# Optimization experiments

Hardware: AMD Instinct MI355X
Metric: run time of the kernel (lower is better)

Reference implementation:

```python
import jax, jax.numpy as jnp
import numpy as np

TEMP = 0.07
LAMBDA_INFONCE = 1.0
LAMBDA_NTXENT = 0.5
EPS = 1e-8

B, S, H, C = 32, 2048, 1024, 5


def _l2norm(x):
    # F.normalize-style row L2 normalization
    n = jnp.sqrt(jnp.sum(x * x, axis=1, keepdims=True))
    return x / jnp.maximum(n, 1e-12)


def _proj(x, W1, b1, W2, b2):
    h = jax.nn.relu(x @ W1 + b1)
    return _l2norm(h @ W2 + b2)


def setup_inputs() -> dict:
    key = jax.random.key(0)
    ks = jax.random.split(key, 12)
    sc1 = 1.0 / np.sqrt(H)
    sc2 = 1.0 / np.sqrt(H // 2)
    sc3 = 1.0 / np.sqrt(2 * H)
    return {
        "span_features": jax.random.normal(ks[0], (B, S, H), jnp.float32),
        "aspect_logits": jax.random.normal(ks[1], (B, S, C), jnp.float32),
        "opinion_logits": jax.random.normal(ks[2], (B, S, C), jnp.float32),
        "sentiment_labels": jax.random.randint(ks[3], (B,), 0, 3),
        "Wa1": jax.random.normal(ks[4], (H, H // 2), jnp.float32) * sc1,
        "ba1": jnp.zeros((H // 2,), jnp.float32),
        "Wa2": jax.random.normal(ks[5], (H // 2, 128), jnp.float32) * sc2,
        "ba2": jnp.zeros((128,), jnp.float32),
        "Wo1": jax.random.normal(ks[6], (H, H // 2), jnp.float32) * sc1,
        "bo1": jnp.zeros((H // 2,), jnp.float32),
        "Wo2": jax.random.normal(ks[7], (H // 2, 128), jnp.float32) * sc2,
        "bo2": jnp.zeros((128,), jnp.float32),
        "Ws1": jax.random.normal(ks[8], (2 * H, H), jnp.float32) * sc3,
        "bs1": jnp.zeros((H,), jnp.float32),
        "Ws2": jax.random.normal(ks[9], (H, 256), jnp.float32) * sc1,
        "bs2": jnp.zeros((256,), jnp.float32),
    }


def _pool(span_features, logits):
    # attention pooling: softmax over seq of summed non-O class logits
    w = jax.nn.softmax(logits[:, :, 1:].sum(axis=-1), axis=-1)  # [B, S]
    return jnp.einsum("bsh,bs->bh", span_features, w)  # [B, H]


def _infonce(a, o, labels):
    n = a.shape[0]
    sim = (a @ o.T) / TEMP  # [B, B]
    same = labels[:, None] == labels[None, :]
    eye = jnp.eye(n, dtype=a.dtype)
    pos_mask = eye + 0.5 * (same & (eye == 0)).astype(a.dtype)
    exp_sim = jnp.exp(sim)
    return -jnp.mean(jnp.log((exp_sim * pos_mask).sum(1) / exp_sim.sum(1) + EPS))


def _ntxent(s, labels):
    n = s.shape[0]
    s = _l2norm(s)
    sim = (s @ s.T) / TEMP
    same = (labels[:, None] == labels[None, :]).astype(s.dtype)
    mask = same - jnp.eye(n, dtype=s.dtype)
    exp_sim = jnp.exp(sim)
    pos = (exp_sim * mask).sum(1)
    neg = (exp_sim * (1.0 - mask)).sum(1)
    pos_count = mask.sum(1)
    has_pos = pos_count > 0
    row = jnp.where(has_pos,
                    -jnp.log(pos / (pos + neg) + EPS) / jnp.maximum(pos_count, 1.0),
                    0.0)
    return row.sum() / jnp.maximum(has_pos.sum(), 1).astype(s.dtype)


def reference(span_features, aspect_logits, opinion_logits, sentiment_labels,
              Wa1, ba1, Wa2, ba2, Wo1, bo1, Wo2, bo2, Ws1, bs1, Ws2, bs2):
    a_emb = _pool(span_features, aspect_logits)   # [B, H]
    o_emb = _pool(span_features, opinion_logits)  # [B, H]
    a_proj = _proj(a_emb, Wa1, ba1, Wa2, ba2)     # [B, 128]
    o_proj = _proj(o_emb, Wo1, bo1, Wo2, bo2)     # [B, 128]
    infonce = _infonce(a_proj, o_proj, sentiment_labels)
    s_proj = _proj(jnp.concatenate([a_emb, o_emb], axis=-1), Ws1, bs1, Ws2, bs2)
    ntxent = _ntxent(s_proj, sentiment_labels)
    # generation_embeddings is None -> cross_modal_loss = 0
    return LAMBDA_INFONCE * infonce + LAMBDA_NTXENT * ntxent
```

## Files before the change

### kernel.cpp

```cpp
#include <hip/hip_runtime.h>
#include <hip/hip_bf16.h>

#define BB 32
#define SS 2048
#define HH 1024
#define CC 5
#define TEMP_INV (1.0f/0.07f)

__global__ void pool_weights(const float* __restrict__ alog,
                             const float* __restrict__ olog,
                             float* __restrict__ w_a,
                             float* __restrict__ w_o) {
    int b = blockIdx.x >> 1;
    int which = blockIdx.x & 1;
    const float* lg = which ? olog : alog;
    float* wout = which ? w_o : w_a;
    __shared__ float raw[SS * CC];
    __shared__ float sl[SS];
    __shared__ float red[256];
    int t = threadIdx.x;
    const float4* src = (const float4*)(lg + (size_t)b * SS * CC);
    float4* dst = (float4*)raw;
    for (int i = t; i < SS * CC / 4; i += 256) dst[i] = src[i];
    __syncthreads();
    for (int s = t; s < SS; s += 256) {
        int base = s * 5;
        sl[s] = raw[base + 1] + raw[base + 2] + raw[base + 3] + raw[base + 4];
    }
    __syncthreads();
    float m = -1e30f;
    for (int s = t; s < SS; s += 256) m = fmaxf(m, sl[s]);
    red[t] = m;
    __syncthreads();
    for (int o = 128; o > 0; o >>= 1) {
        if (t < o) red[t] = fmaxf(red[t], red[t + o]);
        __syncthreads();
    }
    m = red[0];
    __syncthreads();
    float sum = 0.f;
    for (int s = t; s < SS; s += 256) {
        float e = expf(sl[s] - m);
        sl[s] = e;
        sum += e;
    }
    red[t] = sum;
    __syncthreads();
    for (int o = 128; o > 0; o >>= 1) {
        if (t < o) red[t] += red[t + o];
        __syncthreads();
    }
    float inv = 1.0f / red[0];
    for (int s = t; s < SS; s += 256) wout[(size_t)b * SS + s] = sl[s] * inv;
}

__global__ void pool_partial(const float* __restrict__ span,
                             const float* __restrict__ w_a,
                             const float* __restrict__ w_o,
                             float* __restrict__ part_a,
                             float* __restrict__ part_o) {
    int b = blockIdx.x >> 5;
    int chunk = blockIdx.x & 31;
    int t = threadIdx.x;
    __shared__ float wa[64], wo[64];
    int s0 = chunk * 64;
    if (t < 64) {
        wa[t] = w_a[(size_t)b * SS + s0 + t];
        wo[t] = w_o[(size_t)b * SS + s0 + t];
    }
    __syncthreads();
    const float4* sp = (const float4*)span + ((size_t)b * SS + s0) * (HH / 4) + t;
    float4 aa = {0.f, 0.f, 0.f, 0.f};
    float4 oo = {0.f, 0.f, 0.f, 0.f};
    #pragma unroll 8
    for (int ss = 0; ss < 64; ++ss) {
        float4 v = sp[(size_t)ss * (HH / 4)];
        float fa = wa[ss], fo = wo[ss];
        aa.x += v.x * fa; aa.y += v.y * fa; aa.z += v.z * fa; aa.w += v.w * fa;
        oo.x += v.x * fo; oo.y += v.y * fo; oo.z += v.z * fo; oo.w += v.w * fo;
    }
    size_t idx = ((size_t)chunk * BB + b) * HH + (size_t)t * 4;
    *(float4*)(part_a + idx) = aa;
    *(float4*)(part_o + idx) = oo;
}

__global__ void pool_reduce(const float* __restrict__ part_a,
                            const float* __restrict__ part_o,
                            float* __restrict__ a_emb,
                            float* __restrict__ o_emb) {
    int gid = blockIdx.x * 256 + threadIdx.x;
    int which = gid >> 15;
    int r = gid & 32767;
    const float* p = which ? part_o : part_a;
    float s = 0.f;
    #pragma unroll
    for (int c = 0; c < 32; ++c) s += p[(size_t)c * 32768 + r];
    (which ? o_emb : a_emb)[r] = s;
}

__global__ void gemm1_all(const float* __restrict__ a_emb, const float* __restrict__ o_emb,
                          const float* __restrict__ Wa1, const float* __restrict__ Wo1,
                          const float* __restrict__ Ws1,
                          float* __restrict__ p1_a, float* __restrict__ p1_o,
                          float* __restrict__ p1_s) {
    int bid = blockIdx.x;
    const float* xp; const float* W; float* part; int N, kb, jb;
    if (bid < 32) {
        jb = bid & 7; kb = bid >> 3; N = 512; W = Wa1; part = p1_a;
        xp = a_emb + kb * 256;
    } else if (bid < 64) {
        int r = bid - 32;
        jb = r & 7; kb = r >> 3; N = 512; W = Wo1; part = p1_o;
        xp = o_emb + kb * 256;
    } else {
        int r = bid - 64;
        jb = r & 15; kb = r >> 4; N = 1024; W = Ws1; part = p1_s;
        int kk0 = kb * 256;
        xp = (kk0 < 1024) ? (a_emb + kk0) : (o_emb + (kk0 - 1024));
    }
    int k0 = kb * 256;
    __shared__ float xs[32][256];
    int t = threadIdx.x;
    #pragma unroll
    for (int i = 0; i < 8; ++i) {
        int f = t + i * 256;
        int b = f >> 6;
        int kk = (f & 63) * 4;
        *(float4*)(&xs[b][kk]) = *(const float4*)(xp + (size_t)b * HH + kk);
    }
    __syncthreads();
    int jl = t & 63, bg = t >> 6;
    int j = jb * 64 + jl;
    float acc[8] = {0.f, 0.f, 0.f, 0.f, 0.f, 0.f, 0.f, 0.f};
    const float* Wp = W + (size_t)k0 * N + j;
    for (int k = 0; k < 256; k += 4) {
        float w0 = Wp[(size_t)(k + 0) * N];
        float w1 = Wp[(size_t)(k + 1) * N];
        float w2 = Wp[(size_t)(k + 2) * N];
        float w3 = Wp[(size_t)(k + 3) * N];
        #pragma unroll
        for (int bi = 0; bi < 8; ++bi) {
            float4 xv = *(const float4*)(&xs[bg * 8 + bi][k]);
            acc[bi] += xv.x * w0 + xv.y * w1 + xv.z * w2 + xv.w * w3;
        }
    }
    float* pp = part + (size_t)kb * 32 * N + j;
    #pragma unroll
    for (int bi = 0; bi < 8; ++bi)
        pp[(size_t)(bg * 8 + bi) * N] = acc[bi];
}

__global__ void layer2_all(const float* __restrict__ p1_a, const float* __restrict__ ba1,
                           const float* __restrict__ Wa2, const float* __restrict__ ba2,
                           const float* __restrict__ p1_o, const float* __restrict__ bo1,
                           const float* __restrict__ Wo2, const float* __restrict__ bo2,
                           const float* __restrict__ p1_s, const float* __restrict__ bs1,
                           const float* __restrict__ Ws2, const float* __restrict__ bs2,
                           float* __restrict__ a_proj, float* __restrict__ o_proj,
                           float* __restrict__ s_proj) {
    __shared__ float x[1024];
    __shared__ float red[256];
    int bid = blockIdx.x;
    int t = threadIdx.x;
    if (bid < 64) {
        int which = bid >> 5;
        int b = bid & 31;
        const float* part = which ? p1_o : p1_a;
        const float* b1 = which ? bo1 : ba1;
        const float* W2 = which ? Wo2 : Wa2;
        const float* b2 = which ? bo2 : ba2;
        float* out = (which ? o_proj : a_proj) + (size_t)b * 128;
        for (int j = t; j < 512; j += 256) {
            float s = b1[j];
            #pragma unroll
            for (int kb = 0; kb < 4; ++kb) s += part[(size_t)kb * 32 * 512 + (size_t)b * 512 + j];
            x[j] = fmaxf(s, 0.f);
        }
        __syncthreads();
        float acc = 0.f;
        if (t < 128) {
            acc = b2[t];
            for (int k = 0; k < 512; ++k) acc += x[k] * W2[(size_t)k * 128 + t];
        }
        red[t] = (t < 128) ? acc * acc : 0.f;
        __syncthreads();
        for (int o = 128; o > 0; o >>= 1) {
            if (t < o) red[t] += red[t + o];
            __syncthreads();
        }
        float n = fmaxf(sqrtf(red[0]), 1e-12f);
        if (t < 128) out[t] = acc / n;
    } else {
        int b = bid - 64;
        for (int j = t; j < 1024; j += 256) {
            float s = bs1[j];
            #pragma unroll
            for (int kb = 0; kb < 8; ++kb) s += p1_s[(size_t)kb * 32 * 1024 + (size_t)b * 1024 + j];
            x[j] = fmaxf(s, 0.f);
        }
        __syncthreads();
        float acc = bs2[t];
        for (int k = 0; k < 1024; ++k) acc += x[k] * Ws2[(size_t)k * 256 + t];
        red[t] = acc * acc;
        __syncthreads();
        for (int o = 128; o > 0; o >>= 1) {
            if (t < o) red[t] += red[t + o];
            __syncthreads();
        }
        float n = fmaxf(sqrtf(red[0]), 1e-12f);
        s_proj[(size_t)b * 256 + t] = acc / n;
    }
}

__global__ void loss_kernel(const float* __restrict__ a_proj,
                            const float* __restrict__ o_proj,
                            const float* __restrict__ s_proj,
                            const int* __restrict__ labels,
                            float* __restrict__ out) {
    __shared__ float ap[BB * 128];
    __shared__ float op[BB * 128];
    __shared__ float sp[BB * 256];
    __shared__ float rowv[BB], rownt[BB];
    __shared__ int hp[BB], lab[BB];
    int t = threadIdx.x;
    for (int i = t; i < BB * 128; i += 1024) { ap[i] = a_proj[i]; op[i] = o_proj[i]; }
    for (int i = t; i < BB * 256; i += 1024) sp[i] = s_proj[i];
    if (t < BB) lab[t] = labels[t];
    __syncthreads();
    int i = t >> 5, j = t & 31;

    float ssq = 0.f;
    for (int k = 0; k < 8; ++k) {
        float v = sp[i * 256 + j * 8 + k];
        ssq += v * v;
    }
    for (int m = 16; m > 0; m >>= 1) ssq += __shfl_xor(ssq, m, 64);
    float inv = 1.0f / fmaxf(sqrtf(ssq), 1e-12f);
    for (int k = j; k < 256; k += 32) sp[i * 256 + k] *= inv;
    __syncthreads();

    float dot = 0.f;
    for (int k = 0; k < 128; ++k) dot += ap[i * 128 + k] * op[j * 128 + k];
    float e = expf(dot * TEMP_INV);
    float maskv = (i == j) ? 1.0f : ((lab[i] == lab[j]) ? 0.5f : 0.0f);
    float num = e * maskv, den = e;
    for (int m = 16; m > 0; m >>= 1) {
        num += __shfl_xor(num, m, 64);
        den += __shfl_xor(den, m, 64);
    }

    float dn = 0.f;
    for (int k = 0; k < 256; ++k) dn += sp[i * 256 + k] * sp[j * 256 + k];
    float en = expf(dn * TEMP_INV);
    float mnt = (lab[i] == lab[j]) ? ((i == j) ? 0.f : 1.f) : 0.f;
    float pos = en * mnt, neg = en * (1.f - mnt), pc = mnt;
    for (int m = 16; m > 0; m >>= 1) {
        pos += __shfl_xor(pos, m, 64);
        neg += __shfl_xor(neg, m, 64);
        pc += __shfl_xor(pc, m, 64);
    }

    if (j == 0) {
        rowv[i] = -logf(num / den + 1e-8f);
        bool has = pc > 0.f;
        rownt[i] = has ? (-logf(pos / (pos + neg) + 1e-8f) / fmaxf(pc, 1.0f)) : 0.f;
        hp[i] = has ? 1 : 0;
    }
    __syncthreads();
    if (t == 0) {
        float inf = 0.f, nt = 0.f;
        int h = 0;
        for (int q = 0; q < BB; ++q) { inf += rowv[q]; nt += rownt[q]; h += hp[q]; }
        inf /= (float)BB;
        nt /= (float)(h > 0 ? h : 1);
        out[0] = 1.0f * inf + 0.5f * nt;
    }
}

extern "C" void kernel_launch(void* const* d_in, const int* in_sizes, int n_in,
                              void* d_out, int out_size, void* d_ws, size_t ws_size,
                              hipStream_t stream) {
    const float* span  = (const float*)d_in[0];
    const float* alog  = (const float*)d_in[1];
    const float* olog  = (const float*)d_in[2];
    const int*   labs  = (const int*)d_in[3];
    const float* Wa1   = (const float*)d_in[4];
    const float* ba1   = (const float*)d_in[5];
    const float* Wa2   = (const float*)d_in[6];
    const float* ba2   = (const float*)d_in[7];
    const float* Wo1   = (const float*)d_in[8];
    const float* bo1   = (const float*)d_in[9];
    const float* Wo2   = (const float*)d_in[10];
    const float* bo2   = (const float*)d_in[11];
    const float* Ws1   = (const float*)d_in[12];
    const float* bs1   = (const float*)d_in[13];
    const float* Ws2   = (const float*)d_in[14];
    const float* bs2   = (const float*)d_in[15];

    float* ws = (float*)d_ws;
    float* w_a    = ws;
    float* w_o    = ws + 65536;
    float* part_a = ws + 131072;
    float* part_o = ws + 1179648;
    float* a_emb  = ws + 2228224;
    float* o_emb  = ws + 2260992;
    float* p1_a   = ws + 2293760;
    float* p1_o   = ws + 2359296;
    float* p1_s   = ws + 2424832;
    float* a_proj = ws + 2686976;
    float* o_proj = ws + 2691072;
    float* s_proj = ws + 2695168;

    hipLaunchKernelGGL(pool_weights, dim3(64), dim3(256), 0, stream, alog, olog, w_a, w_o);
    hipLaunchKernelGGL(pool_partial, dim3(1024), dim3(256), 0, stream,
                       span, w_a, w_o, part_a, part_o);
    hipLaunchKernelGGL(pool_reduce, dim3(256), dim3(256), 0, stream,
                       part_a, part_o, a_emb, o_emb);
    hipLaunchKernelGGL(gemm1_all, dim3(192), dim3(256), 0, stream,
                       a_emb, o_emb, Wa1, Wo1, Ws1, p1_a, p1_o, p1_s);
    hipLaunchKernelGGL(layer2_all, dim3(96), dim3(256), 0, stream,
                       p1_a, ba1, Wa2, ba2, p1_o, bo1, Wo2, bo2,
                       p1_s, bs1, Ws2, bs2, a_proj, o_proj, s_proj);
    hipLaunchKernelGGL(loss_kernel, dim3(1), dim3(1024), 0, stream,
                       a_proj, o_proj, s_proj, labs, (float*)d_out);
}
```

Before: 531.0 us.

## Split tail GEMMs finer across more threads and pad loss-kernel shared arrays

The first projection GEMM now uses K-chunks of 128 instead of 256 with 512-thread blocks and twice as many blocks, so more CUs work on the weight reads. The second layer splits the K dimension across thread groups and combines them in shared memory. The loss kernel pads its shared arrays to avoid bank conflicts in the row-dot loops. All of this targets the small tail kernels, while the dominant cost is the span pooling pass, which is unchanged.

```diff
diff --git a/kernel.cpp b/kernel.cpp
--- a/kernel.cpp
+++ b/kernel.cpp
@@ -7,7 +7,7 @@
 #define CC 5
 #define TEMP_INV (1.0f/0.07f)
 
-__global__ void pool_weights(const float* __restrict__ alog,
+__global__ __launch_bounds__(256) void pool_weights(const float* __restrict__ alog,
                              const float* __restrict__ olog,
                              float* __restrict__ w_a,
                              float* __restrict__ w_o) {
@@ -54,7 +54,7 @@
     for (int s = t; s < SS; s += 256) wout[(size_t)b * SS + s] = sl[s] * inv;
 }
 
-__global__ void pool_partial(const float* __restrict__ span,
+__global__ __launch_bounds__(256) void pool_partial(const float* __restrict__ span,
                              const float* __restrict__ w_a,
                              const float* __restrict__ w_o,
                              float* __restrict__ part_a,
@@ -84,7 +84,7 @@
     *(float4*)(part_o + idx) = oo;
 }
 
-__global__ void pool_reduce(const float* __restrict__ part_a,
+__global__ __launch_bounds__(256) void pool_reduce(const float* __restrict__ part_a,
                             const float* __restrict__ part_o,
                             float* __restrict__ a_emb,
                             float* __restrict__ o_emb) {
@@ -98,59 +98,59 @@
     (which ? o_emb : a_emb)[r] = s;
 }
 
-__global__ void gemm1_all(const float* __restrict__ a_emb, const float* __restrict__ o_emb,
+__global__ __launch_bounds__(512) void gemm1_all(const float* __restrict__ a_emb, const float* __restrict__ o_emb,
                           const float* __restrict__ Wa1, const float* __restrict__ Wo1,
                           const float* __restrict__ Ws1,
                           float* __restrict__ p1_a, float* __restrict__ p1_o,
                           float* __restrict__ p1_s) {
     int bid = blockIdx.x;
     const float* xp; const float* W; float* part; int N, kb, jb;
-    if (bid < 32) {
+    if (bid < 64) {
         jb = bid & 7; kb = bid >> 3; N = 512; W = Wa1; part = p1_a;
-        xp = a_emb + kb * 256;
-    } else if (bid < 64) {
-        int r = bid - 32;
+        xp = a_emb + kb * 128;
+    } else if (bid < 128) {
+        int r = bid - 64;
         jb = r & 7; kb = r >> 3; N = 512; W = Wo1; part = p1_o;
-        xp = o_emb + kb * 256;
+        xp = o_emb + kb * 128;
     } else {
-        int r = bid - 64;
+        int r = bid - 128;
         jb = r & 15; kb = r >> 4; N = 1024; W = Ws1; part = p1_s;
-        int kk0 = kb * 256;
+        int kk0 = kb * 128;
         xp = (kk0 < 1024) ? (a_emb + kk0) : (o_emb + (kk0 - 1024));
     }
-    int k0 = kb * 256;
-    __shared__ float xs[32][256];
+    int k0 = kb * 128;
+    __shared__ float xs[32][128];
     int t = threadIdx.x;
     #pragma unroll
-    for (int i = 0; i < 8; ++i) {
-        int f = t + i * 256;
-        int b = f >> 6;
-        int kk = (f & 63) * 4;
+    for (int i = 0; i < 2; ++i) {
+        int f = t + i * 512;
+        int b = f >> 5;
+        int kk = (f & 31) * 4;
         *(float4*)(&xs[b][kk]) = *(const float4*)(xp + (size_t)b * HH + kk);
     }
     __syncthreads();
     int jl = t & 63, bg = t >> 6;
     int j = jb * 64 + jl;
-    float acc[8] = {0.f, 0.f, 0.f, 0.f, 0.f, 0.f, 0.f, 0.f};
+    float acc[4] = {0.f, 0.f, 0.f, 0.f};
     const float* Wp = W + (size_t)k0 * N + j;
-    for (int k = 0; k < 256; k += 4) {
+    for (int k = 0; k < 128; k += 4) {
         float w0 = Wp[(size_t)(k + 0) * N];
         float w1 = Wp[(size_t)(k + 1) * N];
         float w2 = Wp[(size_t)(k + 2) * N];
         float w3 = Wp[(size_t)(k + 3) * N];
         #pragma unroll
-        for (int bi = 0; bi < 8; ++bi) {
-            float4 xv = *(const float4*)(&xs[bg * 8 + bi][k]);
+        for (int bi = 0; bi < 4; ++bi) {
+            float4 xv = *(const float4*)(&xs[bg * 4 + bi][k]);
             acc[bi] += xv.x * w0 + xv.y * w1 + xv.z * w2 + xv.w * w3;
         }
     }
     float* pp = part + (size_t)kb * 32 * N + j;
     #pragma unroll
-    for (int bi = 0; bi < 8; ++bi)
-        pp[(size_t)(bg * 8 + bi) * N] = acc[bi];
-}
-
-__global__ void layer2_all(const float* __restrict__ p1_a, const float* __restrict__ ba1,
+    for (int bi = 0; bi < 4; ++bi)
+        pp[(size_t)(bg * 4 + bi) * N] = acc[bi];
+}
+
+__global__ __launch_bounds__(512) void layer2_all(const float* __restrict__ p1_a, const float* __restrict__ ba1,
                            const float* __restrict__ Wa2, const float* __restrict__ ba2,
                            const float* __restrict__ p1_o, const float* __restrict__ bo1,
                            const float* __restrict__ Wo2, const float* __restrict__ bo2,
@@ -159,7 +159,7 @@
                            float* __restrict__ a_proj, float* __restrict__ o_proj,
                            float* __restrict__ s_proj) {
     __shared__ float x[1024];
-    __shared__ float red[256];
+    __shared__ float red[512];
     int bid = blockIdx.x;
     int t = threadIdx.x;
     if (bid < 64) {
@@ -170,77 +170,96 @@
         const float* W2 = which ? Wo2 : Wa2;
         const float* b2 = which ? bo2 : ba2;
         float* out = (which ? o_proj : a_proj) + (size_t)b * 128;
-        for (int j = t; j < 512; j += 256) {
-            float s = b1[j];
+        {
+            float s = b1[t];
             #pragma unroll
-            for (int kb = 0; kb < 4; ++kb) s += part[(size_t)kb * 32 * 512 + (size_t)b * 512 + j];
+            for (int kb = 0; kb < 8; ++kb) s += part[(size_t)kb * 32 * 512 + (size_t)b * 512 + t];
+            x[t] = fmaxf(s, 0.f);
+        }
+        __syncthreads();
+        int jj = t & 127, kh = t >> 7;
+        float acc = (kh == 0) ? b2[jj] : 0.f;
+        const float* Wc = W2 + jj;
+        for (int k = kh * 128; k < kh * 128 + 128; ++k) acc += x[k] * Wc[(size_t)k * 128];
+        red[t] = acc;
+        __syncthreads();
+        float tot = 0.f;
+        if (t < 128) tot = red[t] + red[t + 128] + red[t + 256] + red[t + 384];
+        __syncthreads();
+        if (t < 128) red[t] = tot * tot;
+        __syncthreads();
+        for (int o = 64; o > 0; o >>= 1) {
+            if (t < o) red[t] += red[t + o];
+            __syncthreads();
+        }
+        float n = fmaxf(sqrtf(red[0]), 1e-12f);
+        if (t < 128) out[t] = tot / n;
+    } else {
+        int b = bid - 64;
+        for (int j = t; j < 1024; j += 512) {
+            float s = bs1[j];
+            #pragma unroll
+            for (int kb = 0; kb < 16; ++kb) s += p1_s[(size_t)kb * 32 * 1024 + (size_t)b * 1024 + j];
             x[j] = fmaxf(s, 0.f);
         }
         __syncthreads();
-        float acc = 0.f;
-        if (t < 128) {
-            acc = b2[t];
-            for (int k = 0; k < 512; ++k) acc += x[k] * W2[(size_t)k * 128 + t];
-        }
-        red[t] = (t < 128) ? acc * acc : 0.f;
+        int jj = t & 255, kh = t >> 8;
+        float acc = (kh == 0) ? bs2[jj] : 0.f;
+        const float* Wc = Ws2 + jj;
+        for (int k = kh * 512; k < kh * 512 + 512; ++k) acc += x[k] * Wc[(size_t)k * 256];
+        red[t] = acc;
+        __syncthreads();
+        float tot = 0.f;
+        if (t < 256) tot = red[t] + red[t + 256];
+        __syncthreads();
+        if (t < 256) red[t] = tot * tot;
         __syncthreads();
         for (int o = 128; o > 0; o >>= 1) {
             if (t < o) red[t] += red[t + o];
             __syncthreads();
         }
         float n = fmaxf(sqrtf(red[0]), 1e-12f);
-        if (t < 128) out[t] = acc / n;
-    } else {
-        int b = bid - 64;
-        for (int j = t; j < 1024; j += 256) {
-            float s = bs1[j];
-            #pragma unroll
-            for (int kb = 0; kb < 8; ++kb) s += p1_s[(size_t)kb * 32 * 1024 + (size_t)b * 1024 + j];
-            x[j] = fmaxf(s, 0.f);
-        }
-        __syncthreads();
-        float acc = bs2[t];
-        for (int k = 0; k < 1024; ++k) acc += x[k] * Ws2[(size_t)k * 256 + t];
-        red[t] = acc * acc;
-        __syncthreads();
-        for (int o = 128; o > 0; o >>= 1) {
-            if (t < o) red[t] += red[t + o];
-            __syncthreads();
-        }
-        float n = fmaxf(sqrtf(red[0]), 1e-12f);
-        s_proj[(size_t)b * 256 + t] = acc / n;
-    }
-}
-
-__global__ void loss_kernel(const float* __restrict__ a_proj,
+        if (t < 256) s_proj[(size_t)b * 256 + t] = tot / n;
+    }
+}
+
+__global__ __launch_bounds__(1024) void loss_kernel(const float* __restrict__ a_proj,
                             const float* __restrict__ o_proj,
                             const float* __restrict__ s_proj,
                             const int* __restrict__ labels,
                             float* __restrict__ out) {
-    __shared__ float ap[BB * 128];
-    __shared__ float op[BB * 128];
-    __shared__ float sp[BB * 256];
+    __shared__ float ap[BB][129];
+    __shared__ float op[BB][129];
+    __shared__ float sp[BB][257];
     __shared__ float rowv[BB], rownt[BB];
     __shared__ int hp[BB], lab[BB];
     int t = threadIdx.x;
-    for (int i = t; i < BB * 128; i += 1024) { ap[i] = a_proj[i]; op[i] = o_proj[i]; }
-    for (int i = t; i < BB * 256; i += 1024) sp[i] = s_proj[i];
+    for (int idx = t; idx < BB * 128; idx += 1024) {
+        int r = idx >> 7, c = idx & 127;
+        ap[r][c] = a_proj[idx];
+        op[r][c] = o_proj[idx];
+    }
+    for (int idx = t; idx < BB * 256; idx += 1024) {
+        int r = idx >> 8, c = idx & 255;
+        sp[r][c] = s_proj[idx];
+    }
     if (t < BB) lab[t] = labels[t];
     __syncthreads();
     int i = t >> 5, j = t & 31;
 
     float ssq = 0.f;
+    #pragma unroll
     for (int k = 0; k < 8; ++k) {
-        float v = sp[i * 256 + j * 8 + k];
+        float v = sp[i][j * 8 + k];
         ssq += v * v;
     }
     for (int m = 16; m > 0; m >>= 1) ssq += __shfl_xor(ssq, m, 64);
     float inv = 1.0f / fmaxf(sqrtf(ssq), 1e-12f);
-    for (int k = j; k < 256; k += 32) sp[i * 256 + k] *= inv;
+    for (int k = j; k < 256; k += 32) sp[i][k] *= inv;
     __syncthreads();
 
     float dot = 0.f;
-    for (int k = 0; k < 128; ++k) dot += ap[i * 128 + k] * op[j * 128 + k];
+    for (int k = 0; k < 128; ++k) dot += ap[i][k] * op[j][k];
     float e = expf(dot * TEMP_INV);
     float maskv = (i == j) ? 1.0f : ((lab[i] == lab[j]) ? 0.5f : 0.0f);
     float num = e * maskv, den = e;
@@ -250,7 +269,7 @@
     }
 
     float dn = 0.f;
-    for (int k = 0; k < 256; ++k) dn += sp[i * 256 + k] * sp[j * 256 + k];
+    for (int k = 0; k < 256; ++k) dn += sp[i][k] * sp[j][k];
     float en = expf(dn * TEMP_INV);
     float mnt = (lab[i] == lab[j]) ? ((i == j) ? 0.f : 1.f) : 0.f;
     float pos = en * mnt, neg = en * (1.f - mnt), pc = mnt;
@@ -305,20 +324,20 @@
     float* a_emb  = ws + 2228224;
     float* o_emb  = ws + 2260992;
     float* p1_a   = ws + 2293760;
-    float* p1_o   = ws + 2359296;
-    float* p1_s   = ws + 2424832;
-    float* a_proj = ws + 2686976;
-    float* o_proj = ws + 2691072;
-    float* s_proj = ws + 2695168;
+    float* p1_o   = ws + 2424832;
+    float* p1_s   = ws + 2555904;
+    float* a_proj = ws + 3080192;
+    float* o_proj = ws + 3084288;
+    float* s_proj = ws + 3088384;
 
     hipLaunchKernelGGL(pool_weights, dim3(64), dim3(256), 0, stream, alog, olog, w_a, w_o);
     hipLaunchKernelGGL(pool_partial, dim3(1024), dim3(256), 0, stream,
                        span, w_a, w_o, part_a, part_o);
     hipLaunchKernelGGL(pool_reduce, dim3(256), dim3(256), 0, stream,
                        part_a, part_o, a_emb, o_emb);
-    hipLaunchKernelGGL(gemm1_all, dim3(192), dim3(256), 0, stream,
+    hipLaunchKernelGGL(gemm1_all, dim3(384), dim3(512), 0, stream,
                        a_emb, o_emb, Wa1, Wo1, Ws1, p1_a, p1_o, p1_s);
-    hipLaunchKernelGGL(layer2_all, dim3(96), dim3(256), 0, stream,
+    hipLaunchKernelGGL(layer2_all, dim3(96), dim3(512), 0, stream,
                        p1_a, ba1, Wa2, ba2, p1_o, bo1, Wo2, bo2,
                        p1_s, bs1, Ws2, bs2, a_proj, o_proj, s_proj);
     hipLaunchKernelGGL(loss_kernel, dim3(1), dim3(1024), 0, stream,
```

Result: slower. 663.4 us (+24.9%).
